# Kernel optimization log

Measured on AMD Instinct MI355X. Metric: run time of the kernel, lower is better.

## Reference

```python
import jax, jax.numpy as jnp
import numpy as np
from jax import lax

B, T, C = 4, 2048, 1024
E, DFF, TOPK = 8, 4096, 2


def setup_inputs() -> dict:
    key = jax.random.key(0)
    ks = jax.random.split(key, 5)
    scale = 0.02
    x = jax.random.normal(ks[0], (B, T, C), dtype=jnp.float32)
    router_w = jax.random.normal(ks[1], (C, E), dtype=jnp.float32) * scale
    router_b = jnp.zeros((E,), dtype=jnp.float32)
    w1 = jax.random.normal(ks[2], (E, C, DFF), dtype=jnp.float32) * scale
    b1 = jnp.zeros((E, DFF), dtype=jnp.float32)
    w2 = jax.random.normal(ks[3], (E, DFF, C), dtype=jnp.float32) * scale
    b2 = jnp.zeros((E, C), dtype=jnp.float32)
    return {"x": x, "router_w": router_w, "router_b": router_b,
            "w1": w1, "b1": b1, "w2": w2, "b2": b2, "top_k": TOPK}


def reference(x, router_w, router_b, w1, b1, w2, b2, top_k):
    # Router: softmax then top-k (matches torch.topk(F.softmax(logits)))
    logits = jnp.einsum('btc,ce->bte', x, router_w) + router_b   # [B,T,E]
    probs = jax.nn.softmax(logits, axis=-1)
    weights, indices = lax.top_k(probs, top_k)                    # [B,T,k]
    n_exp = w1.shape[0]
    # Combined per-expert weight per token (sum over top-k slots hitting expert j)
    onehot = jax.nn.one_hot(indices, n_exp, dtype=x.dtype)        # [B,T,k,E]
    cw = jnp.sum(weights[..., None] * onehot, axis=-2)            # [B,T,E]
    bsz, seq, dim = x.shape
    flat_x = x.reshape(-1, dim)                                   # [N,C]
    flat_cw = cw.reshape(-1, n_exp)                               # [N,E]
    out = jnp.zeros_like(flat_x)
    for j in range(n_exp):  # fixed small expert loop (dropout=0 -> eval)
        h = jax.nn.gelu(flat_x @ w1[j] + b1[j], approximate=False)
        out = out + flat_cw[:, j:j + 1] * (h @ w2[j] + b2[j])
    return out.reshape(bsz, seq, dim)
```

## Files before the change

kernel.cpp:

```cpp
#include <hip/hip_runtime.h>
#include <math.h>

typedef __bf16 bf16;
typedef bf16 bf16x4 __attribute__((ext_vector_type(4)));
typedef bf16 bf16x8 __attribute__((ext_vector_type(8)));
typedef float f32x4 __attribute__((ext_vector_type(4)));

#define NTOK 8192
#define CDIM 1024
#define EXP 8
#define DFF 4096
#define BM 128
#define BN 128
#define BK 32

__device__ __forceinline__ void gld_lds16(const bf16* g, bf16* l) {
  __builtin_amdgcn_global_load_lds(
      (const __attribute__((address_space(1))) unsigned int*)g,
      (__attribute__((address_space(3))) unsigned int*)l, 16, 0, 0);
}

__global__ __launch_bounds__(256) void transpose_cvt(
    const float* __restrict__ in, bf16* __restrict__ out, int R, int Cin) {
  __shared__ float tile[32][33];
  int e = blockIdx.z;
  const float* ip = in + (size_t)e * R * Cin;
  bf16* op = out + (size_t)e * R * Cin;
  int c0 = blockIdx.x * 32, r0 = blockIdx.y * 32;
  int tx = threadIdx.x & 31, ty = threadIdx.x >> 5;
#pragma unroll
  for (int i = 0; i < 4; i++)
    tile[ty + 8 * i][tx] = ip[(size_t)(r0 + ty + 8 * i) * Cin + c0 + tx];
  __syncthreads();
#pragma unroll
  for (int i = 0; i < 4; i++)
    op[(size_t)(c0 + ty + 8 * i) * R + r0 + tx] = (bf16)tile[tx][ty + 8 * i];
}

__global__ __launch_bounds__(256) void router_kernel(
    const float* __restrict__ x, const float* __restrict__ rw,
    const float* __restrict__ rb, unsigned int* __restrict__ cnt,
    int* __restrict__ list, float* __restrict__ wq) {
  int wave = threadIdx.x >> 6, lane = threadIdx.x & 63;
  int t = blockIdx.x * 4 + wave;
  if (t >= NTOK) return;
  const float* xr = x + (size_t)t * CDIM;
  float acc[8] = {0.f, 0.f, 0.f, 0.f, 0.f, 0.f, 0.f, 0.f};
  for (int c = lane; c < CDIM; c += 64) {
    float xv = xr[c];
    const float4* rp = (const float4*)(rw + c * 8);
    float4 r0 = rp[0], r1 = rp[1];
    acc[0] += xv * r0.x; acc[1] += xv * r0.y;
    acc[2] += xv * r0.z; acc[3] += xv * r0.w;
    acc[4] += xv * r1.x; acc[5] += xv * r1.y;
    acc[6] += xv * r1.z; acc[7] += xv * r1.w;
  }
#pragma unroll
  for (int e = 0; e < 8; e++)
#pragma unroll
    for (int off = 32; off; off >>= 1) acc[e] += __shfl_down(acc[e], off);
  if (lane == 0) {
    float p[8], mx = -1e30f;
#pragma unroll
    for (int e = 0; e < 8; e++) { p[e] = acc[e] + rb[e]; mx = fmaxf(mx, p[e]); }
    float s = 0.f;
#pragma unroll
    for (int e = 0; e < 8; e++) { p[e] = expf(p[e] - mx); s += p[e]; }
    float inv = 1.0f / s;
#pragma unroll
    for (int e = 0; e < 8; e++) p[e] *= inv;
    int i1 = 0;
#pragma unroll
    for (int e = 1; e < 8; e++) if (p[e] > p[i1]) i1 = e;
    int i2 = (i1 == 0) ? 1 : 0;
#pragma unroll
    for (int e = 0; e < 8; e++) if (e != i1 && p[e] > p[i2]) i2 = e;
    unsigned s0 = atomicAdd(&cnt[i1], 1u);
    list[i1 * NTOK + s0] = t * 2;
    unsigned s1 = atomicAdd(&cnt[i2], 1u);
    list[i2 * NTOK + s1] = t * 2 + 1;
    wq[t * 2] = p[i1];
    wq[t * 2 + 1] = p[i2];
  }
}

__global__ __launch_bounds__(256) void gemm1_kernel(
    const float* __restrict__ x, const bf16* __restrict__ w1b,
    const float* __restrict__ b1, const int* __restrict__ list,
    const unsigned int* __restrict__ cnt, bf16* __restrict__ h) {
  int e = blockIdx.z;
  int count = (int)min(cnt[e], (unsigned)NTOK);
  int m0 = blockIdx.y * BM;
  if (m0 >= count) return;
  int n0 = blockIdx.x * BN;

  __shared__ __align__(16) bf16 As[BM][BK];
  __shared__ __align__(16) bf16 Bs[BN][BK];
  __shared__ int Ls[BM];

  int tid = threadIdx.x;
  if (tid < BM) {
    int gi = m0 + tid;
    Ls[tid] = (gi < count) ? list[e * NTOK + gi] : 0;
  }
  __syncthreads();

  const float* arow[4];
  int arr[4], acol4[4];
#pragma unroll
  for (int p = 0; p < 4; p++) {
    int idx = p * 256 + tid;
    arr[p] = idx >> 3;
    acol4[p] = (idx & 7) * 4;
    arow[p] = x + (size_t)(Ls[arr[p]] >> 1) * CDIM;
  }
  const bf16* brow0 = w1b + (size_t)e * DFF * CDIM +
                      (size_t)(n0 + (tid >> 2)) * CDIM + (tid & 3) * 8;
  const bf16* brow1 = brow0 + (size_t)64 * CDIM;
  bf16* bdst0 = &Bs[tid >> 2][(tid & 3) * 8];
  bf16* bdst1 = &Bs[64 + (tid >> 2)][(tid & 3) * 8];

  f32x4 acc[4][4] = {};
  int wave = tid >> 6, lane = tid & 63;
  int wm = wave & 1, wn = wave >> 1;
  int ln = lane & 15, kq = lane >> 4;

  for (int k0 = 0; k0 < CDIM; k0 += BK) {
    __syncthreads();
    gld_lds16(brow0 + k0, bdst0);
    gld_lds16(brow1 + k0, bdst1);
#pragma unroll
    for (int p = 0; p < 4; p++) {
      float4 v = *(const float4*)(arow[p] + k0 + acol4[p]);
      bf16x4 bv;
      bv[0] = (bf16)v.x; bv[1] = (bf16)v.y; bv[2] = (bf16)v.z; bv[3] = (bf16)v.w;
      *(bf16x4*)&As[arr[p]][acol4[p]] = bv;
    }
    __syncthreads();
    bf16x8 af[4], bfr[4];
#pragma unroll
    for (int i = 0; i < 4; i++)
      af[i] = *(bf16x8*)&As[wm * 64 + i * 16 + ln][kq * 8];
#pragma unroll
    for (int j = 0; j < 4; j++)
      bfr[j] = *(bf16x8*)&Bs[wn * 64 + j * 16 + ln][kq * 8];
#pragma unroll
    for (int i = 0; i < 4; i++)
#pragma unroll
      for (int j = 0; j < 4; j++)
        acc[i][j] = __builtin_amdgcn_mfma_f32_16x16x32_bf16(af[i], bfr[j],
                                                            acc[i][j], 0, 0, 0);
  }
#pragma unroll
  for (int j = 0; j < 4; j++) {
    int n = n0 + wn * 64 + j * 16 + ln;
    float b1v = b1[e * DFF + n];
#pragma unroll
    for (int i = 0; i < 4; i++) {
#pragma unroll
      for (int r = 0; r < 4; r++) {
        int mrow = wm * 64 + i * 16 + kq * 4 + r;
        if (m0 + mrow < count) {
          int enc = Ls[mrow];
          float v = acc[i][j][r] + b1v;
          float g = 0.5f * v * (1.0f + erff(v * 0.70710678118654752f));
          h[(size_t)enc * DFF + n] = (bf16)g;
        }
      }
    }
  }
}

__global__ __launch_bounds__(256) void gemm2_kernel(
    const bf16* __restrict__ h, const bf16* __restrict__ w2b,
    const float* __restrict__ b2, const int* __restrict__ list,
    const unsigned int* __restrict__ cnt, const float* __restrict__ wq,
    float* __restrict__ out) {
  int e = blockIdx.z;
  int count = (int)min(cnt[e], (unsigned)NTOK);
  int m0 = blockIdx.y * BM;
  if (m0 >= count) return;
  int n0 = blockIdx.x * BN;

  __shared__ __align__(16) bf16 As[BM][BK];
  __shared__ __align__(16) bf16 Bs[BN][BK];
  __shared__ int Ls[BM];

  int tid = threadIdx.x;
  if (tid < BM) {
    int gi = m0 + tid;
    Ls[tid] = (gi < count) ? list[e * NTOK + gi] : 0;
  }
  __syncthreads();

  const bf16* arow0 = h + (size_t)Ls[tid >> 2] * DFF + (tid & 3) * 8;
  const bf16* arow1 = h + (size_t)Ls[64 + (tid >> 2)] * DFF + (tid & 3) * 8;
  bf16* adst0 = &As[tid >> 2][(tid & 3) * 8];
  bf16* adst1 = &As[64 + (tid >> 2)][(tid & 3) * 8];
  const bf16* brow0 = w2b + (size_t)e * CDIM * DFF +
                      (size_t)(n0 + (tid >> 2)) * DFF + (tid & 3) * 8;
  const bf16* brow1 = brow0 + (size_t)64 * DFF;
  bf16* bdst0 = &Bs[tid >> 2][(tid & 3) * 8];
  bf16* bdst1 = &Bs[64 + (tid >> 2)][(tid & 3) * 8];

  f32x4 acc[4][4] = {};
  int wave = tid >> 6, lane = tid & 63;
  int wm = wave & 1, wn = wave >> 1;
  int ln = lane & 15, kq = lane >> 4;

  for (int k0 = 0; k0 < DFF; k0 += BK) {
    __syncthreads();
    gld_lds16(arow0 + k0, adst0);
    gld_lds16(arow1 + k0, adst1);
    gld_lds16(brow0 + k0, bdst0);
    gld_lds16(brow1 + k0, bdst1);
    __syncthreads();
    bf16x8 af[4], bfr[4];
#pragma unroll
    for (int i = 0; i < 4; i++)
      af[i] = *(bf16x8*)&As[wm * 64 + i * 16 + ln][kq * 8];
#pragma unroll
    for (int j = 0; j < 4; j++)
      bfr[j] = *(bf16x8*)&Bs[wn * 64 + j * 16 + ln][kq * 8];
#pragma unroll
    for (int i = 0; i < 4; i++)
#pragma unroll
      for (int j = 0; j < 4; j++)
        acc[i][j] = __builtin_amdgcn_mfma_f32_16x16x32_bf16(af[i], bfr[j],
                                                            acc[i][j], 0, 0, 0);
  }
#pragma unroll
  for (int j = 0; j < 4; j++) {
    int n = n0 + wn * 64 + j * 16 + ln;
    float b2v = b2[e * CDIM + n];
#pragma unroll
    for (int i = 0; i < 4; i++) {
#pragma unroll
      for (int r = 0; r < 4; r++) {
        int mrow = wm * 64 + i * 16 + kq * 4 + r;
        if (m0 + mrow < count) {
          int enc = Ls[mrow];
          int t = enc >> 1;
          float w = wq[enc];
          atomicAdd(&out[(size_t)t * CDIM + n], w * (acc[i][j][r] + b2v));
        }
      }
    }
  }
}

extern "C" void kernel_launch(void* const* d_in, const int* in_sizes, int n_in,
                              void* d_out, int out_size, void* d_ws,
                              size_t ws_size, hipStream_t stream) {
  const float* x = (const float*)d_in[0];
  const float* rw = (const float*)d_in[1];
  const float* rb = (const float*)d_in[2];
  const float* w1 = (const float*)d_in[3];
  const float* b1 = (const float*)d_in[4];
  const float* w2 = (const float*)d_in[5];
  const float* b2 = (const float*)d_in[6];
  float* out = (float*)d_out;

  char* ws = (char*)d_ws;
  size_t o = 0;
  auto carve = [&](size_t bytes) {
    void* p = ws + o;
    o = (o + bytes + 255) & ~(size_t)255;
    return p;
  };
  bf16* w1b = (bf16*)carve((size_t)EXP * DFF * CDIM * 2);
  bf16* w2b = (bf16*)carve((size_t)EXP * DFF * CDIM * 2);
  bf16* h = (bf16*)carve((size_t)2 * NTOK * DFF * 2);
  int* list = (int*)carve((size_t)EXP * NTOK * 4);
  float* wq = (float*)carve((size_t)2 * NTOK * 4);
  unsigned int* cnt = (unsigned int*)carve(64);

  hipMemsetAsync(out, 0, (size_t)out_size * sizeof(float), stream);
  hipMemsetAsync(cnt, 0, 64, stream);

  transpose_cvt<<<dim3(DFF / 32, CDIM / 32, EXP), 256, 0, stream>>>(w1, w1b,
                                                                    CDIM, DFF);
  transpose_cvt<<<dim3(CDIM / 32, DFF / 32, EXP), 256, 0, stream>>>(w2, w2b,
                                                                    DFF, CDIM);
  router_kernel<<<NTOK / 4, 256, 0, stream>>>(x, rw, rb, cnt, list, wq);
  gemm1_kernel<<<dim3(DFF / BN, NTOK / BM, EXP), 256, 0, stream>>>(
      x, w1b, b1, list, cnt, h);
  gemm2_kernel<<<dim3(CDIM / BN, NTOK / BM, EXP), 256, 0, stream>>>(
      h, w2b, b2, list, cnt, wq, out);
}
```

Measured before the change: 1.225 ms.

## Pre-convert x to bf16 and load GEMM1 A tiles via direct global-to-LDS

Adds a kernel that converts x to bf16 once, so GEMM1 can gather A rows with global_load_lds like the B tiles instead of loading fp32, converting in registers and storing to LDS on every K step. This halves A-operand bytes per tile and removes per-iteration conversion work from the GEMM inner loop. It also vectorises the transpose_cvt stores to 8-byte bf16x4 writes. The cost is an extra pass over x and an extra workspace buffer.

```diff
diff --git a/kernel.cpp b/kernel.cpp
--- a/kernel.cpp
+++ b/kernel.cpp
@@ -18,6 +18,17 @@
   __builtin_amdgcn_global_load_lds(
       (const __attribute__((address_space(1))) unsigned int*)g,
       (__attribute__((address_space(3))) unsigned int*)l, 16, 0, 0);
+}
+
+__global__ __launch_bounds__(256) void convert_x(const float* __restrict__ in,
+                                                 bf16* __restrict__ out) {
+  int idx = (blockIdx.x * 256 + threadIdx.x) * 8;
+  float4 a = *(const float4*)(in + idx);
+  float4 b = *(const float4*)(in + idx + 4);
+  bf16x8 v;
+  v[0] = (bf16)a.x; v[1] = (bf16)a.y; v[2] = (bf16)a.z; v[3] = (bf16)a.w;
+  v[4] = (bf16)b.x; v[5] = (bf16)b.y; v[6] = (bf16)b.z; v[7] = (bf16)b.w;
+  *(bf16x8*)(out + idx) = v;
 }
 
 __global__ __launch_bounds__(256) void transpose_cvt(
@@ -32,9 +43,13 @@
   for (int i = 0; i < 4; i++)
     tile[ty + 8 * i][tx] = ip[(size_t)(r0 + ty + 8 * i) * Cin + c0 + tx];
   __syncthreads();
-#pragma unroll
-  for (int i = 0; i < 4; i++)
-    op[(size_t)(c0 + ty + 8 * i) * R + r0 + tx] = (bf16)tile[tx][ty + 8 * i];
+  int c = threadIdx.x >> 3, r4 = (threadIdx.x & 7) * 4;
+  bf16x4 v;
+  v[0] = (bf16)tile[r4][c];
+  v[1] = (bf16)tile[r4 + 1][c];
+  v[2] = (bf16)tile[r4 + 2][c];
+  v[3] = (bf16)tile[r4 + 3][c];
+  *(bf16x4*)&op[(size_t)(c0 + c) * R + r0 + r4] = v;
 }
 
 __global__ __launch_bounds__(256) void router_kernel(
@@ -85,7 +100,7 @@
 }
 
 __global__ __launch_bounds__(256) void gemm1_kernel(
-    const float* __restrict__ x, const bf16* __restrict__ w1b,
+    const bf16* __restrict__ xb, const bf16* __restrict__ w1b,
     const float* __restrict__ b1, const int* __restrict__ list,
     const unsigned int* __restrict__ cnt, bf16* __restrict__ h) {
   int e = blockIdx.z;
@@ -105,15 +120,11 @@
   }
   __syncthreads();
 
-  const float* arow[4];
-  int arr[4], acol4[4];
-#pragma unroll
-  for (int p = 0; p < 4; p++) {
-    int idx = p * 256 + tid;
-    arr[p] = idx >> 3;
-    acol4[p] = (idx & 7) * 4;
-    arow[p] = x + (size_t)(Ls[arr[p]] >> 1) * CDIM;
-  }
+  const bf16* arow0 = xb + (size_t)(Ls[tid >> 2] >> 1) * CDIM + (tid & 3) * 8;
+  const bf16* arow1 =
+      xb + (size_t)(Ls[64 + (tid >> 2)] >> 1) * CDIM + (tid & 3) * 8;
+  bf16* adst0 = &As[tid >> 2][(tid & 3) * 8];
+  bf16* adst1 = &As[64 + (tid >> 2)][(tid & 3) * 8];
   const bf16* brow0 = w1b + (size_t)e * DFF * CDIM +
                       (size_t)(n0 + (tid >> 2)) * CDIM + (tid & 3) * 8;
   const bf16* brow1 = brow0 + (size_t)64 * CDIM;
@@ -127,15 +138,10 @@
 
   for (int k0 = 0; k0 < CDIM; k0 += BK) {
     __syncthreads();
+    gld_lds16(arow0 + k0, adst0);
+    gld_lds16(arow1 + k0, adst1);
     gld_lds16(brow0 + k0, bdst0);
     gld_lds16(brow1 + k0, bdst1);
-#pragma unroll
-    for (int p = 0; p < 4; p++) {
-      float4 v = *(const float4*)(arow[p] + k0 + acol4[p]);
-      bf16x4 bv;
-      bv[0] = (bf16)v.x; bv[1] = (bf16)v.y; bv[2] = (bf16)v.z; bv[3] = (bf16)v.w;
-      *(bf16x4*)&As[arr[p]][acol4[p]] = bv;
-    }
     __syncthreads();
     bf16x8 af[4], bfr[4];
 #pragma unroll
@@ -271,6 +277,7 @@
   bf16* w1b = (bf16*)carve((size_t)EXP * DFF * CDIM * 2);
   bf16* w2b = (bf16*)carve((size_t)EXP * DFF * CDIM * 2);
   bf16* h = (bf16*)carve((size_t)2 * NTOK * DFF * 2);
+  bf16* xb = (bf16*)carve((size_t)NTOK * CDIM * 2);
   int* list = (int*)carve((size_t)EXP * NTOK * 4);
   float* wq = (float*)carve((size_t)2 * NTOK * 4);
   unsigned int* cnt = (unsigned int*)carve(64);
@@ -278,13 +285,14 @@
   hipMemsetAsync(out, 0, (size_t)out_size * sizeof(float), stream);
   hipMemsetAsync(cnt, 0, 64, stream);
 
+  convert_x<<<NTOK * CDIM / (256 * 8), 256, 0, stream>>>(x, xb);
   transpose_cvt<<<dim3(DFF / 32, CDIM / 32, EXP), 256, 0, stream>>>(w1, w1b,
                                                                     CDIM, DFF);
   transpose_cvt<<<dim3(CDIM / 32, DFF / 32, EXP), 256, 0, stream>>>(w2, w2b,
                                                                     DFF, CDIM);
   router_kernel<<<NTOK / 4, 256, 0, stream>>>(x, rw, rb, cnt, list, wq);
   gemm1_kernel<<<dim3(DFF / BN, NTOK / BM, EXP), 256, 0, stream>>>(
-      x, w1b, b1, list, cnt, h);
+      xb, w1b, b1, list, cnt, h);
   gemm2_kernel<<<dim3(CDIM / BN, NTOK / BM, EXP), 256, 0, stream>>>(
       h, w2b, b2, list, cnt, wq, out);
 }
```

Result: faster. 1.176 ms (-4.0%).
